# Performance work log

Measured on AMD Instinct MI355X. Metric: run time of the kernel, lower is better.

## Reference

```python
import jax, jax.numpy as jnp
import numpy as np

B, C, H, W = 8, 256, 64, 64
RED = 8
GAMMA = 1.0

def setup_inputs() -> dict:
    key = jax.random.key(0)
    k0, k1, k2, k3 = jax.random.split(key, 4)
    Cr = C // RED
    scale = 1.0 / np.sqrt(C).astype(np.float32)
    x = jax.random.normal(k0, (B, C, H, W), jnp.float32)
    # 1x1 conv weights (no bias) == channel-mixing matrices [out_c, in_c]
    w1 = jax.random.normal(k1, (Cr, C), jnp.float32) * scale  # query proj
    w2 = jax.random.normal(k2, (Cr, C), jnp.float32) * scale  # key proj
    w3 = jax.random.normal(k3, (C, C), jnp.float32) * scale   # value proj
    return {"x": x, "w1": w1, "w2": w2, "w3": w3}

def reference(x, w1, w2, w3):
    b, c, h, w = x.shape
    n = h * w
    xf = x.reshape(b, c, n)                      # [B,C,N]  (hw_flattern)
    f = jnp.einsum('oc,bcn->bon', w1, xf)        # [B,Cr,N] conv1 (1x1)
    g = jnp.einsum('oc,bcn->bon', w2, xf)        # [B,Cr,N] conv2 (1x1)
    hh = jnp.einsum('oc,bcn->bon', w3, xf)       # [B,C,N]  conv3 (1x1)
    # s = f^T g : [B,N,N]
    s = jnp.einsum('bki,bkj->bij', f, g)
    # NOTE: torch softmax over dim=1 (rows), not the usual last dim
    beta = jax.nn.softmax(s, axis=1)             # [B,N,N]
    o = jnp.einsum('bck,bkn->bcn', hh, beta)     # [B,C,N]
    o = o.reshape(b, c, h, w)
    return GAMMA * o + x
```

## Files before the change

### kernel.cpp

```cpp
#include <hip/hip_runtime.h>
#include <stdint.h>

#define Bsz 8
#define Cc  256
#define Crr 32
#define Nn  4096
#define CN  (Cc * Nn)
#define ITILE 128
#define NIT (Nn / ITILE)
#define PPITCH 136
#define YPITCH 264

typedef unsigned short u16;
typedef __attribute__((ext_vector_type(8))) short  short8;
typedef __attribute__((ext_vector_type(4))) float  floatx4;
typedef __attribute__((ext_vector_type(4))) unsigned short u16x4;

__device__ __forceinline__ floatx4 mfma16(short8 a, short8 b, floatx4 c) {
  return __builtin_amdgcn_mfma_f32_16x16x32_bf16(a, b, c, 0, 0, 0);
}
__device__ __forceinline__ u16 f2bf(float f) {
  unsigned int u = __builtin_bit_cast(unsigned int, f);
  u = (u + 0x7FFFu + ((u >> 16) & 1u)) >> 16;
  return (u16)u;
}
__device__ __forceinline__ float bf2f(u16 h) {
  unsigned int u = ((unsigned int)h) << 16;
  return __builtin_bit_cast(float, u);
}
__device__ __forceinline__ short8 pack8(const float* __restrict__ p) {
  floatx4 a = *(const floatx4*)p;
  floatx4 b = *(const floatx4*)(p + 4);
  short8 r;
  r[0] = (short)f2bf(a[0]); r[1] = (short)f2bf(a[1]);
  r[2] = (short)f2bf(a[2]); r[3] = (short)f2bf(a[3]);
  r[4] = (short)f2bf(b[0]); r[5] = (short)f2bf(b[1]);
  r[6] = (short)f2bf(b[2]); r[7] = (short)f2bf(b[3]);
  return r;
}
__device__ __forceinline__ void split8(const float* __restrict__ p,
                                       short8& hi, short8& lo) {
  floatx4 a = *(const floatx4*)p;
  floatx4 b = *(const floatx4*)(p + 4);
  float v[8] = {a[0], a[1], a[2], a[3], b[0], b[1], b[2], b[3]};
#pragma unroll
  for (int r = 0; r < 8; ++r) {
    u16 h = f2bf(v[r]);
    hi[r] = (short)h;
    lo[r] = (short)f2bf(v[r] - bf2f(h));
  }
}

template <bool XB16>
__launch_bounds__(256, 4)
__global__ void proj_kernel(const float* __restrict__ x,
                            const float* __restrict__ w1,
                            const float* __restrict__ w2,
                            const float* __restrict__ w3,
                            u16* __restrict__ w3b,
                            u16* __restrict__ fThi, u16* __restrict__ fTlo,
                            u16* __restrict__ gThi, u16* __restrict__ gTlo,
                            u16* __restrict__ xb) {
  const int bid = blockIdx.x;
  const int b   = bid & 7;
  const int nt  = bid >> 3;
  const int tid  = threadIdx.x;
  const int w    = tid >> 6;
  const int lane = tid & 63;
  const int m    = lane & 15;
  const int q    = lane >> 4;
  const int nb   = nt * 16;

  __shared__ float comb[3][16][64];

  const float* xsl = x + (size_t)b * CN;
  const floatx4 z4 = {0.f, 0.f, 0.f, 0.f};
  floatx4 aF[2] = {z4, z4}, aG[2] = {z4, z4};

  for (int ci = 0; ci < 2; ++ci) {
    const int c0 = w * 64 + ci * 32;
    const float* xp = xsl + (size_t)(c0 + q * 8) * Nn + nb + m;
    short8 xh, xl;
#pragma unroll
    for (int r = 0; r < 8; ++r) {
      float v = xp[(size_t)r * Nn];
      u16 h = f2bf(v);
      xh[r] = (short)h;
      xl[r] = (short)f2bf(v - bf2f(h));
    }
    if (XB16) {
      const int n = nb + m;
      const size_t tb = (size_t)b * CN;
#pragma unroll
      for (int r = 0; r < 8; ++r) {
        int c = c0 + q * 8 + r;
        xb[tb + ((size_t)((n >> 5) * 16 + (c >> 4)) << 9) +
           (c & 15) * 32 + (n & 31)] = (u16)xh[r];
      }
    }
#pragma unroll
    for (int ot = 0; ot < 2; ++ot) {
      short8 wh, wl;
      split8(w1 + (size_t)(ot * 16 + m) * Cc + c0 + q * 8, wh, wl);
      aF[ot] = mfma16(xh, wh, aF[ot]);
      aF[ot] = mfma16(xh, wl, aF[ot]);
      aF[ot] = mfma16(xl, wh, aF[ot]);
      split8(w2 + (size_t)(ot * 16 + m) * Cc + c0 + q * 8, wh, wl);
      aG[ot] = mfma16(xh, wh, aG[ot]);
      aG[ot] = mfma16(xh, wl, aG[ot]);
      aG[ot] = mfma16(xl, wh, aG[ot]);
    }
  }

  if (w > 0) {
#pragma unroll
    for (int k = 0; k < 2; ++k)
#pragma unroll
      for (int r = 0; r < 4; ++r) {
        comb[w - 1][k * 4 + r][lane]     = aF[k][r];
        comb[w - 1][8 + k * 4 + r][lane] = aG[k][r];
      }
  }
  __syncthreads();
  if (w == 0) {
#pragma unroll
    for (int ot = 0; ot < 2; ++ot)
#pragma unroll
      for (int r = 0; r < 4; ++r) {
        float vf = aF[ot][r] + comb[0][ot * 4 + r][lane] +
                   comb[1][ot * 4 + r][lane] + comb[2][ot * 4 + r][lane];
        float vg = aG[ot][r] + comb[0][8 + ot * 4 + r][lane] +
                   comb[1][8 + ot * 4 + r][lane] + comb[2][8 + ot * 4 + r][lane];
        int n = nb + q * 4 + r;
        size_t idx = ((size_t)b * Nn + n) * Crr + ot * 16 + m;
        u16 hf = f2bf(vf);
        fThi[idx] = hf;
        fTlo[idx] = f2bf(vf - bf2f(hf));
        u16 hg = f2bf(vg);
        gThi[idx] = hg;
        gTlo[idx] = f2bf(vg - bf2f(hg));
      }
  }
  if (bid < 64) {
    int base = bid * 1024 + tid * 4;
    floatx4 v = *(const floatx4*)(w3 + base);
    u16x4 o;
    o[0] = f2bf(v[0]); o[1] = f2bf(v[1]); o[2] = f2bf(v[2]); o[3] = f2bf(v[3]);
    *(u16x4*)(w3b + base) = o;
  }
}

template <bool XB16>
__launch_bounds__(512, 4)
__global__ void attn_kernel(const u16* __restrict__ fThi,
                            const u16* __restrict__ fTlo,
                            const u16* __restrict__ gThi,
                            const u16* __restrict__ gTlo,
                            const u16* __restrict__ xb,
                            const float* __restrict__ x,
                            const u16* __restrict__ w3b,
                            float* __restrict__ out) {
  const int bid = blockIdx.x;
  const int b   = bid & 7;
  const int jt  = bid >> 3;
  const int j0  = jt * 64;
  const int tid  = threadIdx.x;
  const int w    = tid >> 6;
  const int lane = tid & 63;
  const int m    = lane & 15;
  const int q    = lane >> 4;

  __shared__ u16   P[2 * 64 * PPITCH];
  __shared__ float lred[32 * 64];
  __shared__ float linv[64];

  const size_t fgb = (size_t)b * (size_t)Nn * Crr;
  const u16*   xbs = xb + (size_t)b * CN;
  const float* xfs = x + (size_t)b * CN;

  short8 bgh[4], bgl[4];
#pragma unroll
  for (int jb = 0; jb < 4; ++jb) {
    size_t idx = fgb + (size_t)(j0 + jb * 16 + m) * Crr + q * 8;
    bgh[jb] = *(const short8*)(gThi + idx);
    bgl[jb] = *(const short8*)(gTlo + idx);
  }

  const floatx4 z4 = {0.f, 0.f, 0.f, 0.f};
  floatx4 acc[2][4];
#pragma unroll
  for (int cb = 0; cb < 2; ++cb)
#pragma unroll
    for (int jb = 0; jb < 4; ++jb) acc[cb][jb] = z4;

  float ps[4] = {0.f, 0.f, 0.f, 0.f};
  unsigned int pw[4][2];
  short8 fAh, fAl, fBh, fBl;

  auto sPart = [&](int jb) {
    floatx4 t3 = mfma16(fAl, bgh[jb], z4);
    t3 = mfma16(fAh, bgl[jb], t3);
    t3 = mfma16(fAh, bgh[jb], t3);
    u16 h0 = f2bf(__expf(t3[0]));
    u16 h1 = f2bf(__expf(t3[1]));
    u16 h2 = f2bf(__expf(t3[2]));
    u16 h3 = f2bf(__expf(t3[3]));
    ps[jb] += (bf2f(h0) + bf2f(h1)) + (bf2f(h2) + bf2f(h3));
    pw[jb][0] = (unsigned int)h0 | ((unsigned int)h1 << 16);
    pw[jb][1] = (unsigned int)h2 | ((unsigned int)h3 << 16);
  };

  {
    size_t fidx = fgb + (size_t)(w * 16 + m) * Crr + q * 8;
    fAh = *(const short8*)(fThi + fidx);
    fAl = *(const short8*)(fTlo + fidx);
#pragma unroll
    for (int jb = 0; jb < 4; ++jb) sPart(jb);
    size_t f1 = fgb + (size_t)(ITILE + w * 16 + m) * Crr + q * 8;
    fAh = *(const short8*)(fThi + f1);
    fAl = *(const short8*)(fTlo + f1);
  }

  const int gr = w * 2 + (q >> 1);
  for (int t = 0; t < NIT - 1; ++t) {
    u16* buf = P + (t & 1) * (64 * PPITCH);
#pragma unroll
    for (int jb = 0; jb < 4; ++jb) {
      const int j = jb * 16 + m;
      *(uint2*)(buf + j * PPITCH + gr * 8 + (q & 1) * 4) =
          make_uint2(pw[jb][0], pw[jb][1]);
    }
    __syncthreads();

    if (t + 2 < NIT) {
      size_t fidx = fgb + (size_t)((t + 2) * ITILE + w * 16 + m) * Crr + q * 8;
      fBh = *(const short8*)(fThi + fidx);
      fBl = *(const short8*)(fTlo + fidx);
    }

#pragma unroll
    for (int kk = 0; kk < 4; ++kk) {
      short8 bp[4];
#pragma unroll
      for (int jb = 0; jb < 4; ++jb)
        bp[jb] = *(const short8*)(buf + (jb * 16 + m) * PPITCH + (kk * 4 + q) * 8);
#pragma unroll
      for (int cb = 0; cb < 2; ++cb) {
        short8 ah;
        if (XB16) {
          const int tile = (t * 4 + kk) * 16 + (w * 2 + cb);
          ah = *(const short8*)(xbs + ((size_t)tile << 9) + m * 32 + q * 8);
        } else {
          ah = pack8(xfs + (size_t)(((w * 2 + cb) * 16 + m)) * Nn +
                     t * ITILE + kk * 32 + q * 8);
        }
#pragma unroll
        for (int jb = 0; jb < 4; ++jb)
          acc[cb][jb] = mfma16(ah, bp[jb], acc[cb][jb]);
      }
      sPart(kk);
    }
    fAh = fBh; fAl = fBl;
  }

  {
    const int t = NIT - 1;
    u16* buf = P + (t & 1) * (64 * PPITCH);
#pragma unroll
    for (int jb = 0; jb < 4; ++jb) {
      const int j = jb * 16 + m;
      *(uint2*)(buf + j * PPITCH + gr * 8 + (q & 1) * 4) =
          make_uint2(pw[jb][0], pw[jb][1]);
    }
    __syncthreads();
#pragma unroll
    for (int kk = 0; kk < 4; ++kk) {
      short8 bp[4];
#pragma unroll
      for (int jb = 0; jb < 4; ++jb)
        bp[jb] = *(const short8*)(buf + (jb * 16 + m) * PPITCH + (kk * 4 + q) * 8);
#pragma unroll
      for (int cb = 0; cb < 2; ++cb) {
        short8 ah;
        if (XB16) {
          const int tile = (t * 4 + kk) * 16 + (w * 2 + cb);
          ah = *(const short8*)(xbs + ((size_t)tile << 9) + m * 32 + q * 8);
        } else {
          ah = pack8(xfs + (size_t)(((w * 2 + cb) * 16 + m)) * Nn +
                     t * ITILE + kk * 32 + q * 8);
        }
#pragma unroll
        for (int jb = 0; jb < 4; ++jb)
          acc[cb][jb] = mfma16(ah, bp[jb], acc[cb][jb]);
      }
    }
  }

#pragma unroll
  for (int jb = 0; jb < 4; ++jb)
    lred[(w * 4 + q) * 64 + jb * 16 + m] = ps[jb];
  __syncthreads();
  if (tid < 64) {
    float s = 0.f;
#pragma unroll
    for (int t2 = 0; t2 < 32; ++t2) s += lred[t2 * 64 + tid];
    linv[tid] = 1.0f / s;
  }
  __syncthreads();

  u16* yt = P;
#pragma unroll
  for (int cb = 0; cb < 2; ++cb)
#pragma unroll
    for (int jb = 0; jb < 4; ++jb) {
      const int j = jb * 16 + m;
      const float li = linv[j];
      unsigned int d0 = (unsigned int)f2bf(acc[cb][jb][0] * li) |
                        ((unsigned int)f2bf(acc[cb][jb][1] * li) << 16);
      unsigned int d1 = (unsigned int)f2bf(acc[cb][jb][2] * li) |
                        ((unsigned int)f2bf(acc[cb][jb][3] * li) << 16);
      *(uint2*)(yt + j * YPITCH + (w * 2 + cb) * 16 + q * 4) = make_uint2(d0, d1);
    }
  __syncthreads();

  floatx4 macc[2][4];
#pragma unroll
  for (int ct = 0; ct < 2; ++ct)
#pragma unroll
    for (int jb = 0; jb < 4; ++jb) macc[ct][jb] = z4;

  for (int k0 = 0; k0 < Cc; k0 += 32) {
    short8 bf_[4];
#pragma unroll
    for (int jb = 0; jb < 4; ++jb)
      bf_[jb] = *(const short8*)(yt + (jb * 16 + m) * YPITCH + k0 + q * 8);
#pragma unroll
    for (int ct = 0; ct < 2; ++ct) {
      short8 aw = *(const short8*)(w3b + (size_t)((w * 2 + ct) * 16 + m) * Cc +
                                   k0 + q * 8);
#pragma unroll
      for (int jb = 0; jb < 4; ++jb)
        macc[ct][jb] = mfma16(aw, bf_[jb], macc[ct][jb]);
    }
  }

  float* osl = out + (size_t)b * CN;
#pragma unroll
  for (int ct = 0; ct < 2; ++ct)
#pragma unroll
    for (int jb = 0; jb < 4; ++jb)
#pragma unroll
      for (int r = 0; r < 4; ++r) {
        const int c = (w * 2 + ct) * 16 + q * 4 + r;
        const size_t idx = (size_t)c * Nn + j0 + jb * 16 + m;
        osl[idx] = macc[ct][jb][r] + xfs[idx];
      }
}

extern "C" void kernel_launch(void* const* d_in, const int* in_sizes, int n_in,
                              void* d_out, int out_size, void* d_ws, size_t ws_size,
                              hipStream_t stream) {
  const float* x  = (const float*)d_in[0];
  const float* w1 = (const float*)d_in[1];
  const float* w2 = (const float*)d_in[2];
  const float* w3 = (const float*)d_in[3];
  float* out = (float*)d_out;

  const size_t FG = (size_t)Bsz * Nn * Crr;
  u16* w3b  = (u16*)d_ws;
  u16* fThi = w3b + (size_t)Cc * Cc;
  u16* fTlo = fThi + FG;
  u16* gThi = fTlo + FG;
  u16* gTlo = gThi + FG;
  u16* xb   = gTlo + FG;
  const size_t need_xb = ((size_t)Cc * Cc + 4 * FG + (size_t)Bsz * CN) * 2;
  const bool use_xb = ws_size >= need_xb;

  if (use_xb) {
    proj_kernel<true><<<dim3(2048), dim3(256), 0, stream>>>(
        x, w1, w2, w3, w3b, fThi, fTlo, gThi, gTlo, xb);
    attn_kernel<true><<<dim3(512), dim3(512), 0, stream>>>(
        fThi, fTlo, gThi, gTlo, xb, x, w3b, out);
  } else {
    proj_kernel<false><<<dim3(2048), dim3(256), 0, stream>>>(
        x, w1, w2, w3, w3b, fThi, fTlo, gThi, gTlo, xb);
    attn_kernel<false><<<dim3(512), dim3(512), 0, stream>>>(
        fThi, fTlo, gThi, gTlo, xb, x, w3b, out);
  }
}
```

Before: 216.0 us.

## Stage x tile through LDS in projection kernel and shuffle-reduce row sums

The projection kernel now loads a 256x32 slab of x into padded LDS with coalesced float4 reads. The bf16 xb tiled copy is written from LDS with 16-byte vector stores, replacing scattered 2-byte stores. Waves are split into two n-halves and two c-halves with a two-way LDS reduction, and the grid is halved to 1024 blocks. The attention kernel reduces softmax column sums with warp shuffles before going to LDS, shrinking the lred buffer, and its launch bound is raised to 8 blocks per CU, which could force register spills. The proj kernel's larger LDS footprint (about 33 KB) may lower its occupancy.

```diff
diff --git a/kernel.cpp b/kernel.cpp
--- a/kernel.cpp
+++ b/kernel.cpp
@@ -15,6 +15,7 @@
 typedef __attribute__((ext_vector_type(8))) short  short8;
 typedef __attribute__((ext_vector_type(4))) float  floatx4;
 typedef __attribute__((ext_vector_type(4))) unsigned short u16x4;
+typedef __attribute__((ext_vector_type(4))) unsigned int uint4v;
 
 __device__ __forceinline__ floatx4 mfma16(short8 a, short8 b, floatx4 c) {
   return __builtin_amdgcn_mfma_f32_16x16x32_bf16(a, b, c, 0, 0, 0);
@@ -69,34 +70,55 @@
   const int lane = tid & 63;
   const int m    = lane & 15;
   const int q    = lane >> 4;
-  const int nb   = nt * 16;
-
-  __shared__ float comb[3][16][64];
+  const int nhalf = w >> 1;
+  const int chalf = w & 1;
+  const int nb0  = nt * 32;
+
+  __shared__ float lds[256 * 33];
 
   const float* xsl = x + (size_t)b * CN;
+
+  {
+    const int row0 = tid >> 3;
+    const int col  = (tid & 7) * 4;
+#pragma unroll
+    for (int rr = 0; rr < 8; ++rr) {
+      const int row = rr * 32 + row0;
+      floatx4 v = *(const floatx4*)(xsl + (size_t)row * Nn + nb0 + col);
+      float* d = &lds[row * 33 + col];
+      d[0] = v[0]; d[1] = v[1]; d[2] = v[2]; d[3] = v[3];
+    }
+  }
+  __syncthreads();
+
+  if (XB16) {
+    u16* xbp = xb + (size_t)b * CN + (size_t)nt * 8192;
+#pragma unroll
+    for (int rr = 0; rr < 4; ++rr) {
+      const int off = (rr * 256 + tid) * 8;
+      const int c  = (off >> 9) * 16 + ((off >> 5) & 15);
+      const int ln = off & 31;
+      const float* src = &lds[c * 33 + ln];
+      uint4v d;
+#pragma unroll
+      for (int e = 0; e < 4; ++e)
+        d[e] = (unsigned int)f2bf(src[2 * e]) |
+               ((unsigned int)f2bf(src[2 * e + 1]) << 16);
+      *(uint4v*)(xbp + off) = d;
+    }
+  }
+
   const floatx4 z4 = {0.f, 0.f, 0.f, 0.f};
   floatx4 aF[2] = {z4, z4}, aG[2] = {z4, z4};
-
-  for (int ci = 0; ci < 2; ++ci) {
-    const int c0 = w * 64 + ci * 32;
-    const float* xp = xsl + (size_t)(c0 + q * 8) * Nn + nb + m;
+  for (int ci = 0; ci < 4; ++ci) {
+    const int c0 = chalf * 128 + ci * 32;
     short8 xh, xl;
 #pragma unroll
     for (int r = 0; r < 8; ++r) {
-      float v = xp[(size_t)r * Nn];
+      float v = lds[(c0 + q * 8 + r) * 33 + nhalf * 16 + m];
       u16 h = f2bf(v);
       xh[r] = (short)h;
       xl[r] = (short)f2bf(v - bf2f(h));
-    }
-    if (XB16) {
-      const int n = nb + m;
-      const size_t tb = (size_t)b * CN;
-#pragma unroll
-      for (int r = 0; r < 8; ++r) {
-        int c = c0 + q * 8 + r;
-        xb[tb + ((size_t)((n >> 5) * 16 + (c >> 4)) << 9) +
-           (c & 15) * 32 + (n & 31)] = (u16)xh[r];
-      }
     }
 #pragma unroll
     for (int ot = 0; ot < 2; ++ot) {
@@ -111,27 +133,26 @@
       aG[ot] = mfma16(xl, wh, aG[ot]);
     }
   }
-
-  if (w > 0) {
-#pragma unroll
-    for (int k = 0; k < 2; ++k)
+  __syncthreads();
+
+  if (chalf) {
+#pragma unroll
+    for (int ot = 0; ot < 2; ++ot)
 #pragma unroll
       for (int r = 0; r < 4; ++r) {
-        comb[w - 1][k * 4 + r][lane]     = aF[k][r];
-        comb[w - 1][8 + k * 4 + r][lane] = aG[k][r];
+        lds[nhalf * 1024 + (ot * 4 + r) * 64 + lane]     = aF[ot][r];
+        lds[nhalf * 1024 + (8 + ot * 4 + r) * 64 + lane] = aG[ot][r];
       }
   }
   __syncthreads();
-  if (w == 0) {
+  if (!chalf) {
 #pragma unroll
     for (int ot = 0; ot < 2; ++ot)
 #pragma unroll
       for (int r = 0; r < 4; ++r) {
-        float vf = aF[ot][r] + comb[0][ot * 4 + r][lane] +
-                   comb[1][ot * 4 + r][lane] + comb[2][ot * 4 + r][lane];
-        float vg = aG[ot][r] + comb[0][8 + ot * 4 + r][lane] +
-                   comb[1][8 + ot * 4 + r][lane] + comb[2][8 + ot * 4 + r][lane];
-        int n = nb + q * 4 + r;
+        float vf = aF[ot][r] + lds[nhalf * 1024 + (ot * 4 + r) * 64 + lane];
+        float vg = aG[ot][r] + lds[nhalf * 1024 + (8 + ot * 4 + r) * 64 + lane];
+        int n = nb0 + nhalf * 16 + q * 4 + r;
         size_t idx = ((size_t)b * Nn + n) * Crr + ot * 16 + m;
         u16 hf = f2bf(vf);
         fThi[idx] = hf;
@@ -151,7 +172,7 @@
 }
 
 template <bool XB16>
-__launch_bounds__(512, 4)
+__launch_bounds__(512, 8)
 __global__ void attn_kernel(const u16* __restrict__ fThi,
                             const u16* __restrict__ fTlo,
                             const u16* __restrict__ gThi,
@@ -171,7 +192,7 @@
   const int q    = lane >> 4;
 
   __shared__ u16   P[2 * 64 * PPITCH];
-  __shared__ float lred[32 * 64];
+  __shared__ float lred[8 * 64];
   __shared__ float linv[64];
 
   const size_t fgb = (size_t)b * (size_t)Nn * Crr;
@@ -297,13 +318,22 @@
   }
 
 #pragma unroll
-  for (int jb = 0; jb < 4; ++jb)
-    lred[(w * 4 + q) * 64 + jb * 16 + m] = ps[jb];
+  for (int jb = 0; jb < 4; ++jb) {
+    float v = ps[jb];
+    v += __shfl_xor(v, 16);
+    v += __shfl_xor(v, 32);
+    ps[jb] = v;
+  }
+  if (q == 0) {
+#pragma unroll
+    for (int jb = 0; jb < 4; ++jb)
+      lred[w * 64 + jb * 16 + m] = ps[jb];
+  }
   __syncthreads();
   if (tid < 64) {
     float s = 0.f;
 #pragma unroll
-    for (int t2 = 0; t2 < 32; ++t2) s += lred[t2 * 64 + tid];
+    for (int t2 = 0; t2 < 8; ++t2) s += lred[t2 * 64 + tid];
     linv[tid] = 1.0f / s;
   }
   __syncthreads();
@@ -377,12 +407,12 @@
   const bool use_xb = ws_size >= need_xb;
 
   if (use_xb) {
-    proj_kernel<true><<<dim3(2048), dim3(256), 0, stream>>>(
+    proj_kernel<true><<<dim3(1024), dim3(256), 0, stream>>>(
         x, w1, w2, w3, w3b, fThi, fTlo, gThi, gTlo, xb);
     attn_kernel<true><<<dim3(512), dim3(512), 0, stream>>>(
         fThi, fTlo, gThi, gTlo, xb, x, w3b, out);
   } else {
-    proj_kernel<false><<<dim3(2048), dim3(256), 0, stream>>>(
+    proj_kernel<false><<<dim3(1024), dim3(256), 0, stream>>>(
         x, w1, w2, w3, w3b, fThi, fTlo, gThi, gTlo, xb);
     attn_kernel<false><<<dim3(512), dim3(512), 0, stream>>>(
         fThi, fTlo, gThi, gTlo, xb, x, w3b, out);
```

Measured after the change: 634.9 us. 2.94x slower.
